# Kernel optimization log

Measured on AMD Instinct MI355X. Metric: run time of the kernel, lower is better.

## Reference

```python
import jax, jax.numpy as jnp
import numpy as np
from jax import lax

DIM = 512
HEADS = 8


def _branch(x, w1, wd):
    # 1x1 pointwise conv (no bias)
    y = jnp.einsum('oc,bchw->bohw', w1, x)
    # ReflectionPad2d(2)
    y = jnp.pad(y, ((0, 0), (0, 0), (2, 2), (2, 2)), mode='reflect')
    # depthwise 3x3, dilation 2, valid padding (net: same spatial size)
    y = lax.conv_general_dilated(
        y, wd, window_strides=(1, 1), padding='VALID', rhs_dilation=(2, 2),
        dimension_numbers=('NCHW', 'OIHW', 'NCHW'), feature_group_count=y.shape[1])
    return y


def setup_inputs() -> dict:
    key = jax.random.key(0)
    ks = jax.random.split(key, 8)
    s = 0.02
    style_feat = jax.random.normal(ks[0], (16, DIM, 64, 64), dtype=jnp.float32)
    fw1 = jax.random.normal(ks[1], (DIM, DIM), dtype=jnp.float32) * s
    fwd_ = jax.random.normal(ks[2], (DIM, 1, 3, 3), dtype=jnp.float32) * s
    gw1 = jax.random.normal(ks[3], (DIM, DIM), dtype=jnp.float32) * s
    gwd = jax.random.normal(ks[4], (DIM, 1, 3, 3), dtype=jnp.float32) * s
    hw1 = jax.random.normal(ks[5], (DIM, DIM), dtype=jnp.float32) * s
    hwd = jax.random.normal(ks[6], (DIM, 1, 3, 3), dtype=jnp.float32) * s
    ow = jax.random.normal(ks[7], (DIM, DIM), dtype=jnp.float32) * s
    temperature = jnp.ones((HEADS, 1, 1), dtype=jnp.float32)
    return dict(style_feat=style_feat, fw1=fw1, fwd_=fwd_, gw1=gw1, gwd=gwd,
                hw1=hw1, hwd=hwd, ow=ow, temperature=temperature)


def reference(style_feat, fw1, fwd_, gw1, gwd, hw1, hwd, ow, temperature):
    B, C, H, W = style_feat.shape
    cph = C // HEADS
    f_x = _branch(style_feat, fw1, fwd_)
    g_x = _branch(style_feat, gw1, gwd)
    h_x = _branch(style_feat, hw1, hwd)
    q = f_x.reshape(B, HEADS, cph, H * W)
    k = g_x.reshape(B, HEADS, cph, H * W)
    v = h_x.reshape(B, HEADS, cph, H * W)
    # channel-wise attention: [B,h,cph,cph]
    energy = jnp.einsum('bhcn,bhdn->bhcd', q, k)
    attn = jax.nn.softmax(energy * temperature[None], axis=-1)
    out = jnp.einsum('bhcd,bhdn->bhcn', attn, v).reshape(B, C, H, W)
    out = jnp.einsum('oc,bchw->bohw', ow, out)
    return out + style_feat
```

## Files before the change

kernel.cpp:

```cpp
#include <hip/hip_runtime.h>

typedef unsigned short u16;
typedef __bf16 bf8_t __attribute__((ext_vector_type(8)));
typedef short short8 __attribute__((ext_vector_type(8)));
typedef u16 u16x4 __attribute__((ext_vector_type(4)));
typedef float f32x4 __attribute__((ext_vector_type(4)));

#define DEV __device__ __forceinline__

DEV u16 f2bf(float x) {
  unsigned u = __builtin_bit_cast(unsigned, x);
  return (u16)((u + 0x7FFFu + ((u >> 16) & 1u)) >> 16);
}
DEV float bf2f(u16 x) {
  unsigned u = (unsigned)x << 16;
  return __builtin_bit_cast(float, u);
}

DEV void gload16(const u16* g, u16* l) {
  __builtin_amdgcn_global_load_lds((__attribute__((address_space(1))) void*)(g),
                                   (__attribute__((address_space(3))) void*)(l), 16, 0, 0);
}

__global__ void k_waw(const float* __restrict__ f, const float* __restrict__ g,
                      const float* __restrict__ h, u16* __restrict__ AW) {
  int cid = blockIdx.x * 256 + threadIdx.x;
  int lane = cid & 63, m = (cid >> 6) & 3, wm = (cid >> 8) & 1;
  int kt = (cid >> 9) & 15, mt = cid >> 13;
  int row = mt * 128 + wm * 64 + m * 16 + (lane & 15);
  int col = kt * 32 + (lane >> 4) * 8;
  int t = row >> 9, rr = row & 511;
  const float* src = (t == 0 ? f : t == 1 ? g : h) + (size_t)rr * 512 + col;
  f32x4 v0 = *(const f32x4*)src;
  f32x4 v1 = *(const f32x4*)(src + 4);
  short8 s;
#pragma unroll
  for (int e = 0; e < 4; ++e) { s[e] = (short)f2bf(v0[e]); s[e + 4] = (short)f2bf(v1[e]); }
  *(short8*)(AW + (size_t)cid * 8) = s;
}

__global__ __launch_bounds__(256) void k_xt(const float* __restrict__ style, u16* __restrict__ Xt) {
  __shared__ float t[32][33];
  int b = blockIdx.z, c0 = blockIdx.y * 32, n0 = blockIdx.x * 32;
  int tid = threadIdx.x, lr = tid >> 5, lc = tid & 31;
  const float* src = style + ((size_t)b * 512 + c0) * 4096 + n0;
#pragma unroll
  for (int it = 0; it < 4; ++it) {
    int r = it * 8 + lr;
    t[r][lc] = src[(size_t)r * 4096 + lc];
  }
  __syncthreads();
  u16* dst = Xt + ((size_t)b * 4096 + n0) * 512 + c0;
#pragma unroll
  for (int it = 0; it < 4; ++it) {
    int n = it * 8 + lr;
    dst[(size_t)n * 512 + lc] = f2bf(t[lc][n]);
  }
}

DEV void stage_tile(const u16* __restrict__ src, int row0, int kb,
                    u16* lds, int wave, int lane) {
#pragma unroll
  for (int qq = 0; qq < 2; ++qq) {
    int idx = (wave * 2 + qq) * 64 + lane;
    int r = idx >> 2;
    int cb = (idx & 3) * 8;
    gload16(src + (size_t)(row0 + r) * 512 + (kb + cb),
            lds + (wave * 2 + qq) * 512);
  }
}

__global__ __launch_bounds__(256, 2) void k_gemm_branch(
    const u16* __restrict__ AW, const u16* __restrict__ Xt, u16* __restrict__ Y) {
  int z = blockIdx.z;
  int t = z >> 4, b = z & 15;
  int mt = t * 4 + blockIdx.y;
  int N0 = blockIdx.x * 128;
  const u16* B = Xt + (size_t)b * (4096 * 512);
  u16* C = Y + (size_t)b * (1536 * 4096);
  int tid = threadIdx.x, wave = tid >> 6, lane = tid & 63;
  int wm = wave >> 1, wn = wave & 1;
  __shared__ __align__(16) u16 lB[2][128 * 32];
  f32x4 acc[4][4];
#pragma unroll
  for (int m = 0; m < 4; ++m)
#pragma unroll
    for (int n = 0; n < 4; ++n) acc[m][n] = (f32x4){0.f, 0.f, 0.f, 0.f};
  stage_tile(B, N0, 0, &lB[0][0], wave, lane);
  __syncthreads();
  int lrow = lane & 15, lk = (lane >> 4) * 8;
#pragma unroll 2
  for (int kt = 0; kt < 16; ++kt) {
    int cur = kt & 1;
    if (kt < 15) stage_tile(B, N0, (kt + 1) * 32, &lB[cur ^ 1][0], wave, lane);
    const u16* ab = AW + (size_t)((mt * 16 + kt) * 2 + wm) * 2048 + lane * 8;
    bf8_t af[4], bff[4];
#pragma unroll
    for (int m = 0; m < 4; ++m) af[m] = *(const bf8_t*)(ab + m * 512);
#pragma unroll
    for (int n = 0; n < 4; ++n)
      bff[n] = *(const bf8_t*)&lB[cur][(wn * 64 + n * 16 + lrow) * 32 + lk];
#pragma unroll
    for (int m = 0; m < 4; ++m)
#pragma unroll
      for (int n = 0; n < 4; ++n)
        acc[m][n] = __builtin_amdgcn_mfma_f32_16x16x32_bf16(af[m], bff[n], acc[m][n], 0, 0, 0);
    __syncthreads();
  }
  int orow = (lane >> 4) * 4, ocol = lane & 15;
#pragma unroll
  for (int m = 0; m < 4; ++m)
#pragma unroll
    for (int n = 0; n < 4; ++n) {
      int row = mt * 128 + wm * 64 + m * 16 + orow;
      int col = N0 + wn * 64 + n * 16 + ocol;
      u16* cp = C + (size_t)row * 4096 + col;
#pragma unroll
      for (int i = 0; i < 4; ++i) cp[(size_t)i * 4096] = f2bf(acc[m][n][i]);
    }
}

template <typename F>
DEV void dw_row(const u16* plane, const float* w9, int y, F&& store) {
  short8 raw[3][8];
#pragma unroll
  for (int i = 0; i < 3; ++i) {
    int yy = y + 2 * i - 2;
    yy = yy < 0 ? -yy : (yy > 63 ? 126 - yy : yy);
    const short8* rp = (const short8*)(plane + yy * 64);
#pragma unroll
    for (int ch = 0; ch < 8; ++ch) raw[i][ch] = rp[ch];
  }
#pragma unroll
  for (int g = 0; g < 4; ++g) {
    float fr[3][20];
#pragma unroll
    for (int t = 0; t < 20; ++t) {
      int p = g * 16 - 2 + t;
      int rp2 = p < 0 ? -p : (p > 63 ? 126 - p : p);
#pragma unroll
      for (int i = 0; i < 3; ++i)
        fr[i][t] = bf2f((u16)raw[i][rp2 >> 3][rp2 & 7]);
    }
    float o[16];
#pragma unroll
    for (int e = 0; e < 16; ++e) {
      float s = 0.f;
#pragma unroll
      for (int i = 0; i < 3; ++i)
#pragma unroll
        for (int j = 0; j < 3; ++j)
          s += w9[i * 3 + j] * fr[i][e + 2 * j];
      o[e] = s;
    }
    store(g, o);
  }
}

__global__ __launch_bounds__(256, 2) void k_dwE(const u16* __restrict__ Y,
    const float* __restrict__ fwd, const float* __restrict__ gwd, float* __restrict__ E) {
  int band = blockIdx.x, h = blockIdx.y, b = blockIdx.z;
  __shared__ __align__(16) u16 qbuf[64 * 256];
  __shared__ __align__(16) u16 kbuf[64 * 256];
  int tid = threadIdx.x;
  int c = ((tid >> 5) << 3) | (tid & 7);
  int yl = (tid >> 3) & 3;
  int wv = tid >> 6, lane = tid & 63;
  int lrow = lane & 15, lkg = lane >> 4;
  const u16* qp = Y + ((size_t)b * 1536 + h * 64 + c) * 4096;
  const u16* kp = Y + ((size_t)b * 1536 + 512 + h * 64 + c) * 4096;
  float wq9[9], wk9[9];
#pragma unroll
  for (int t = 0; t < 9; ++t) {
    wq9[t] = fwd[(h * 64 + c) * 9 + t];
    wk9[t] = gwd[(h * 64 + c) * 9 + t];
  }
  f32x4 acc[4];
#pragma unroll
  for (int n = 0; n < 4; ++n) acc[n] = (f32x4){0.f, 0.f, 0.f, 0.f};
  char* qrow = (char*)qbuf + c * 512;
  char* krow = (char*)kbuf + c * 512;
  int c7 = c & 7;
#pragma unroll 1
  for (int sb = 0; sb < 4; ++sb) {
    int y = band * 16 + sb * 4 + yl;
    dw_row(qp, wq9, y, [&](int g, const float* o) {
      short8 s0, s1;
#pragma unroll
      for (int e = 0; e < 8; ++e) { s0[e] = (short)f2bf(o[e]); s1[e] = (short)f2bf(o[e + 8]); }
      int ch0 = yl * 8 + g * 2;
      *(short8*)(qrow + 16 * (ch0 ^ c7)) = s0;
      *(short8*)(qrow + 16 * ((ch0 + 1) ^ c7)) = s1;
    });
    dw_row(kp, wk9, y, [&](int g, const float* o) {
      short8 s0, s1;
#pragma unroll
      for (int e = 0; e < 8; ++e) { s0[e] = (short)f2bf(o[e]); s1[e] = (short)f2bf(o[e + 8]); }
      int ch0 = yl * 8 + g * 2;
      *(short8*)(krow + 16 * (ch0 ^ c7)) = s0;
      *(short8*)(krow + 16 * ((ch0 + 1) ^ c7)) = s1;
    });
    __syncthreads();
    const char* qb = (const char*)qbuf + (wv * 16 + lrow) * 512;
    int ca7 = (wv * 16 + lrow) & 7;
#pragma unroll
    for (int ks = 0; ks < 8; ++ks) {
      bf8_t aF = *(const bf8_t*)(qb + 16 * ((ks * 4 + lkg) ^ ca7));
#pragma unroll
      for (int n = 0; n < 4; ++n) {
        int cb = n * 16 + lrow;
        bf8_t bF = *(const bf8_t*)((const char*)kbuf + cb * 512 + 16 * ((ks * 4 + lkg) ^ (cb & 7)));
        acc[n] = __builtin_amdgcn_mfma_f32_16x16x32_bf16(aF, bF, acc[n], 0, 0, 0);
      }
    }
    __syncthreads();
  }
  float* Eo = E + (((size_t)band * 16 + b) * 8 + h) * 4096;
  int orow = (lane >> 4) * 4, ocol = lane & 15;
#pragma unroll
  for (int n = 0; n < 4; ++n)
#pragma unroll
    for (int i = 0; i < 4; ++i)
      Eo[(wv * 16 + orow + i) * 64 + n * 16 + ocol] = acc[n][i];
}

__global__ __launch_bounds__(256, 2) void k_dwV(const u16* __restrict__ Y,
    const float* __restrict__ hwd, u16* __restrict__ Vt) {
  int band = blockIdx.x, ct = blockIdx.y, b = blockIdx.z;
  __shared__ float vb[256 * 68];
  int tid = threadIdx.x;
  int c = ((tid >> 5) << 3) | (tid & 7);
  int yl = (tid >> 3) & 3;
  int cg = tid & 7;
  int cglob = ct * 64 + c;
  const u16* plane = Y + ((size_t)b * 1536 + 1024 + cglob) * 4096;
  float w9[9];
#pragma unroll
  for (int t = 0; t < 9; ++t) w9[t] = hwd[cglob * 9 + t];
#pragma unroll 1
  for (int sb = 0; sb < 4; ++sb) {
    int y = band * 16 + sb * 4 + yl;
    dw_row(plane, w9, y, [&](int g, const float* o) {
#pragma unroll
      for (int e = 0; e < 16; ++e)
        vb[((g * 16 + e) * 4 + yl) * 68 + c] = o[e];
    });
    __syncthreads();
#pragma unroll
    for (int k = 0; k < 8; ++k) {
      int np = (tid >> 3) + 32 * k;
      int x = np >> 2, yy = np & 3;
      int ng = (band * 16 + sb * 4 + yy) * 64 + x;
      f32x4 r0 = *(const f32x4*)&vb[np * 68 + cg * 8];
      f32x4 r1 = *(const f32x4*)&vb[np * 68 + cg * 8 + 4];
      short8 s;
#pragma unroll
      for (int e = 0; e < 4; ++e) { s[e] = (short)f2bf(r0[e]); s[e + 4] = (short)f2bf(r1[e]); }
      *(short8*)(Vt + ((size_t)b * 4096 + ng) * 512 + ct * 64 + cg * 8) = s;
    }
    __syncthreads();
  }
}

__global__ __launch_bounds__(64) void k_softmax(float* __restrict__ E, const float* __restrict__ temp) {
  int bh = blockIdx.x;
  int b = bh >> 3, h = bh & 7;
  int c = threadIdx.x;
  float* p0 = E + (((size_t)b * 8 + h) * 64 + c) * 64;
  float tv = temp[h];
  float e[64];
  float mx = -1e30f;
#pragma unroll
  for (int d = 0; d < 64; ++d) {
    float v = (p0[d] + p0[d + 524288] + p0[d + 1048576] + p0[d + 1572864]) * tv;
    e[d] = v;
    mx = fmaxf(mx, v);
  }
  float s = 0.f;
#pragma unroll
  for (int d = 0; d < 64; ++d) { float v = __expf(e[d] - mx); e[d] = v; s += v; }
  float inv = 1.f / s;
#pragma unroll
  for (int d = 0; d < 64; ++d) p0[d] = e[d] * inv;
}

__global__ __launch_bounds__(256) void k_m2(const float* __restrict__ E, const float* __restrict__ ow,
                                            u16* __restrict__ M2) {
  int og = blockIdx.x, h = blockIdx.y, b = blockIdx.z;
  __shared__ float at[4096];
  int tid = threadIdx.x;
  const float* attn = E + ((size_t)b * 8 + h) * 4096;
  for (int v = tid; v < 4096; v += 256) at[v] = attn[v];
  __syncthreads();
  int o = og * 64 + (tid >> 2), dq = (tid & 3) * 16;
  const float* owr = ow + (size_t)o * 512 + h * 64;
  float acc[16];
#pragma unroll
  for (int e = 0; e < 16; ++e) acc[e] = 0.f;
  for (int cc = 0; cc < 64; ++cc) {
    float wv = owr[cc];
#pragma unroll
    for (int e = 0; e < 16; ++e) acc[e] += wv * at[cc * 64 + dq + e];
  }
  u16* dst = M2 + ((size_t)b * 512 + o) * 512 + h * 64 + dq;
  short8 s0, s1;
#pragma unroll
  for (int e = 0; e < 8; ++e) { s0[e] = (short)f2bf(acc[e]); s1[e] = (short)f2bf(acc[e + 8]); }
  *(short8*)dst = s0;
  *(short8*)(dst + 8) = s1;
}

DEV void stage_tile_f(const u16* __restrict__ src, int row0, int kb,
                      u16* lds, int wave, int lane) {
#pragma unroll
  for (int qq = 0; qq < 2; ++qq) {
    int idx = (wave * 2 + qq) * 64 + lane;
    int r = idx >> 2;
    int cb = (idx & 3) * 8;
    gload16(src + (size_t)(row0 + r) * 512 + (kb + cb),
            lds + (wave * 2 + qq) * 512);
  }
}

__global__ __launch_bounds__(256, 2) void k_gemm_final(
    const u16* __restrict__ M2, const u16* __restrict__ Vt,
    const float* __restrict__ style, float* __restrict__ out) {
  int b = blockIdx.z;
  const u16* A = M2 + (size_t)b * (512 * 512);
  const u16* B = Vt + (size_t)b * (4096 * 512);
  const float* st = style + (size_t)b * (512 * 4096);
  float* op = out + (size_t)b * (512 * 4096);
  int M0 = blockIdx.y * 128, N0 = blockIdx.x * 128;
  int tid = threadIdx.x, wave = tid >> 6, lane = tid & 63;
  int wm = wave >> 1, wn = wave & 1;
  __shared__ __align__(16) u16 lA[2][128 * 32];
  __shared__ __align__(16) u16 lB[2][128 * 32];
  f32x4 acc[4][4];
#pragma unroll
  for (int m = 0; m < 4; ++m)
#pragma unroll
    for (int n = 0; n < 4; ++n) acc[m][n] = (f32x4){0.f, 0.f, 0.f, 0.f};
  stage_tile_f(A, M0, 0, &lA[0][0], wave, lane);
  stage_tile_f(B, N0, 0, &lB[0][0], wave, lane);
  __syncthreads();
  int lrow = lane & 15, lk = (lane >> 4) * 8;
#pragma unroll 2
  for (int kt = 0; kt < 16; ++kt) {
    int cur = kt & 1;
    if (kt < 15) {
      stage_tile_f(A, M0, (kt + 1) * 32, &lA[cur ^ 1][0], wave, lane);
      stage_tile_f(B, N0, (kt + 1) * 32, &lB[cur ^ 1][0], wave, lane);
    }
    bf8_t af[4], bff[4];
#pragma unroll
    for (int m = 0; m < 4; ++m)
      af[m] = *(const bf8_t*)&lA[cur][(wm * 64 + m * 16 + lrow) * 32 + lk];
#pragma unroll
    for (int n = 0; n < 4; ++n)
      bff[n] = *(const bf8_t*)&lB[cur][(wn * 64 + n * 16 + lrow) * 32 + lk];
#pragma unroll
    for (int m = 0; m < 4; ++m)
#pragma unroll
      for (int n = 0; n < 4; ++n)
        acc[m][n] = __builtin_amdgcn_mfma_f32_16x16x32_bf16(af[m], bff[n], acc[m][n], 0, 0, 0);
    __syncthreads();
  }
  int orow = (lane >> 4) * 4, ocol = lane & 15;
#pragma unroll
  for (int m = 0; m < 4; ++m)
#pragma unroll
    for (int n = 0; n < 4; ++n) {
      int row = M0 + wm * 64 + m * 16 + orow;
      int col = N0 + wn * 64 + n * 16 + ocol;
      float* cp = op + (size_t)row * 4096 + col;
      const float* sp = st + (size_t)row * 4096 + col;
#pragma unroll
      for (int i = 0; i < 4; ++i) cp[(size_t)i * 4096] = acc[m][n][i] + sp[(size_t)i * 4096];
    }
}


extern "C" void kernel_launch(void* const* d_in, const int* in_sizes, int n_in,
                              void* d_out, int out_size, void* d_ws, size_t ws_size,
                              hipStream_t stream) {
  const float* style = (const float*)d_in[0];
  const float* fw1   = (const float*)d_in[1];
  const float* fwd_  = (const float*)d_in[2];
  const float* gw1   = (const float*)d_in[3];
  const float* gwd   = (const float*)d_in[4];
  const float* hw1   = (const float*)d_in[5];
  const float* hwd   = (const float*)d_in[6];
  const float* ow    = (const float*)d_in[7];
  const float* temp  = (const float*)d_in[8];
  float* out = (float*)d_out;

  char* ws = (char*)d_ws;
  u16*   AW  = (u16*)(ws + 0);
  u16*   Y   = (u16*)(ws + (size_t)2097152);
  u16*   Xt  = (u16*)(ws + (size_t)203423744);
  u16*   Vt  = Xt;
  float* E   = (float*)(ws + (size_t)270532608);
  u16*   M2  = (u16*)(ws + (size_t)278921216);

  k_waw<<<384, 256, 0, stream>>>(fw1, gw1, hw1, AW);
  k_xt<<<dim3(128, 16, 16), 256, 0, stream>>>(style, Xt);
  k_gemm_branch<<<dim3(32, 4, 48), 256, 0, stream>>>(AW, Xt, Y);
  k_dwE<<<dim3(4, 8, 16), 256, 0, stream>>>(Y, fwd_, gwd, E);
  k_dwV<<<dim3(4, 8, 16), 256, 0, stream>>>(Y, hwd, Vt);
  k_softmax<<<128, 64, 0, stream>>>(E, temp);
  k_m2<<<dim3(8, 8, 16), 256, 0, stream>>>(E, ow, M2);
  k_gemm_final<<<dim3(32, 4, 16), 256, 0, stream>>>(M2, Vt, style, out);
}
```

Measured before the change: 413.4 us.

## Stage GEMM epilogue through LDS and fuse dw/softmax kernels

The branch GEMM epilogue now writes its accumulators into a swizzled LDS tile and stores 16-byte coalesced rows, where before it issued scattered 2-byte global stores. The QK-energy and V depthwise kernels are merged into one launch selected by blockIdx.y, so the two sets of blocks run together. Softmax is folded into the M2 kernel, which recomputes the softmax for each output-group block, removing one launch and an E round trip. In exchange, the softmax work is repeated 8 times, the epilogue adds LDS use and barriers, and the larger shared footprint may reduce occupancy.

```diff
diff --git a/kernel.cpp b/kernel.cpp
--- a/kernel.cpp
+++ b/kernel.cpp
@@ -81,6 +81,7 @@
   int tid = threadIdx.x, wave = tid >> 6, lane = tid & 63;
   int wm = wave >> 1, wn = wave & 1;
   __shared__ __align__(16) u16 lB[2][128 * 32];
+  __shared__ __align__(16) u16 Cs[64 * 128];
   f32x4 acc[4][4];
 #pragma unroll
   for (int m = 0; m < 4; ++m)
@@ -109,15 +110,28 @@
   }
   int orow = (lane >> 4) * 4, ocol = lane & 15;
 #pragma unroll
-  for (int m = 0; m < 4; ++m)
-#pragma unroll
-    for (int n = 0; n < 4; ++n) {
-      int row = mt * 128 + wm * 64 + m * 16 + orow;
-      int col = N0 + wn * 64 + n * 16 + ocol;
-      u16* cp = C + (size_t)row * 4096 + col;
-#pragma unroll
-      for (int i = 0; i < 4; ++i) cp[(size_t)i * 4096] = f2bf(acc[m][n][i]);
-    }
+  for (int half = 0; half < 2; ++half) {
+    if (wm == half) {
+#pragma unroll
+      for (int m = 0; m < 4; ++m)
+#pragma unroll
+        for (int n = 0; n < 4; ++n)
+#pragma unroll
+          for (int i = 0; i < 4; ++i) {
+            int r = m * 16 + orow + i;
+            int cph = wn * 64 + n * 16 + ocol;
+            Cs[r * 128 + (((cph >> 3) ^ (r & 15)) << 3) + (cph & 7)] = f2bf(acc[m][n][i]);
+          }
+    }
+    __syncthreads();
+#pragma unroll
+    for (int p = 0; p < 4; ++p) {
+      int r2 = p * 16 + (tid >> 4), g2 = tid & 15;
+      short8 v = *(const short8*)&Cs[r2 * 128 + ((g2 ^ (r2 & 15)) << 3)];
+      *(short8*)(C + (size_t)(mt * 128 + half * 64 + r2) * 4096 + N0 + g2 * 8) = v;
+    }
+    if (half == 0) __syncthreads();
+  }
 }
 
 template <typename F>
@@ -157,140 +171,136 @@
   }
 }
 
-__global__ __launch_bounds__(256, 2) void k_dwE(const u16* __restrict__ Y,
-    const float* __restrict__ fwd, const float* __restrict__ gwd, float* __restrict__ E) {
-  int band = blockIdx.x, h = blockIdx.y, b = blockIdx.z;
-  __shared__ __align__(16) u16 qbuf[64 * 256];
-  __shared__ __align__(16) u16 kbuf[64 * 256];
+__global__ __launch_bounds__(256, 2) void k_dw2(const u16* __restrict__ Y,
+    const float* __restrict__ fwd, const float* __restrict__ gwd,
+    const float* __restrict__ hwd, float* __restrict__ E, u16* __restrict__ Vt) {
+  __shared__ __align__(16) char smem[69632];
+  int band = blockIdx.x, b = blockIdx.z;
   int tid = threadIdx.x;
-  int c = ((tid >> 5) << 3) | (tid & 7);
-  int yl = (tid >> 3) & 3;
-  int wv = tid >> 6, lane = tid & 63;
-  int lrow = lane & 15, lkg = lane >> 4;
-  const u16* qp = Y + ((size_t)b * 1536 + h * 64 + c) * 4096;
-  const u16* kp = Y + ((size_t)b * 1536 + 512 + h * 64 + c) * 4096;
-  float wq9[9], wk9[9];
-#pragma unroll
-  for (int t = 0; t < 9; ++t) {
-    wq9[t] = fwd[(h * 64 + c) * 9 + t];
-    wk9[t] = gwd[(h * 64 + c) * 9 + t];
-  }
-  f32x4 acc[4];
-#pragma unroll
-  for (int n = 0; n < 4; ++n) acc[n] = (f32x4){0.f, 0.f, 0.f, 0.f};
-  char* qrow = (char*)qbuf + c * 512;
-  char* krow = (char*)kbuf + c * 512;
-  int c7 = c & 7;
+  if (blockIdx.y < 8) {
+    int h = blockIdx.y;
+    u16* qbuf = (u16*)smem;
+    u16* kbuf = (u16*)(smem + 32768);
+    int c = ((tid >> 5) << 3) | (tid & 7);
+    int yl = (tid >> 3) & 3;
+    int wv = tid >> 6, lane = tid & 63;
+    int lrow = lane & 15, lkg = lane >> 4;
+    const u16* qp = Y + ((size_t)b * 1536 + h * 64 + c) * 4096;
+    const u16* kp = Y + ((size_t)b * 1536 + 512 + h * 64 + c) * 4096;
+    float wq9[9], wk9[9];
+#pragma unroll
+    for (int t = 0; t < 9; ++t) {
+      wq9[t] = fwd[(h * 64 + c) * 9 + t];
+      wk9[t] = gwd[(h * 64 + c) * 9 + t];
+    }
+    f32x4 acc[4];
+#pragma unroll
+    for (int n = 0; n < 4; ++n) acc[n] = (f32x4){0.f, 0.f, 0.f, 0.f};
+    char* qrow = (char*)qbuf + c * 512;
+    char* krow = (char*)kbuf + c * 512;
+    int c7 = c & 7;
 #pragma unroll 1
-  for (int sb = 0; sb < 4; ++sb) {
-    int y = band * 16 + sb * 4 + yl;
-    dw_row(qp, wq9, y, [&](int g, const float* o) {
-      short8 s0, s1;
-#pragma unroll
-      for (int e = 0; e < 8; ++e) { s0[e] = (short)f2bf(o[e]); s1[e] = (short)f2bf(o[e + 8]); }
-      int ch0 = yl * 8 + g * 2;
-      *(short8*)(qrow + 16 * (ch0 ^ c7)) = s0;
-      *(short8*)(qrow + 16 * ((ch0 + 1) ^ c7)) = s1;
-    });
-    dw_row(kp, wk9, y, [&](int g, const float* o) {
-      short8 s0, s1;
-#pragma unroll
-      for (int e = 0; e < 8; ++e) { s0[e] = (short)f2bf(o[e]); s1[e] = (short)f2bf(o[e + 8]); }
-      int ch0 = yl * 8 + g * 2;
-      *(short8*)(krow + 16 * (ch0 ^ c7)) = s0;
-      *(short8*)(krow + 16 * ((ch0 + 1) ^ c7)) = s1;
-    });
-    __syncthreads();
-    const char* qb = (const char*)qbuf + (wv * 16 + lrow) * 512;
-    int ca7 = (wv * 16 + lrow) & 7;
-#pragma unroll
-    for (int ks = 0; ks < 8; ++ks) {
-      bf8_t aF = *(const bf8_t*)(qb + 16 * ((ks * 4 + lkg) ^ ca7));
-#pragma unroll
-      for (int n = 0; n < 4; ++n) {
-        int cb = n * 16 + lrow;
-        bf8_t bF = *(const bf8_t*)((const char*)kbuf + cb * 512 + 16 * ((ks * 4 + lkg) ^ (cb & 7)));
-        acc[n] = __builtin_amdgcn_mfma_f32_16x16x32_bf16(aF, bF, acc[n], 0, 0, 0);
+    for (int sb = 0; sb < 4; ++sb) {
+      int y = band * 16 + sb * 4 + yl;
+      dw_row(qp, wq9, y, [&](int g, const float* o) {
+        short8 s0, s1;
+#pragma unroll
+        for (int e = 0; e < 8; ++e) { s0[e] = (short)f2bf(o[e]); s1[e] = (short)f2bf(o[e + 8]); }
+        int ch0 = yl * 8 + g * 2;
+        *(short8*)(qrow + 16 * (ch0 ^ c7)) = s0;
+        *(short8*)(qrow + 16 * ((ch0 + 1) ^ c7)) = s1;
+      });
+      dw_row(kp, wk9, y, [&](int g, const float* o) {
+        short8 s0, s1;
+#pragma unroll
+        for (int e = 0; e < 8; ++e) { s0[e] = (short)f2bf(o[e]); s1[e] = (short)f2bf(o[e + 8]); }
+        int ch0 = yl * 8 + g * 2;
+        *(short8*)(krow + 16 * (ch0 ^ c7)) = s0;
+        *(short8*)(krow + 16 * ((ch0 + 1) ^ c7)) = s1;
+      });
+      __syncthreads();
+      const char* qb = (const char*)qbuf + (wv * 16 + lrow) * 512;
+      int ca7 = (wv * 16 + lrow) & 7;
+#pragma unroll
+      for (int ks = 0; ks < 8; ++ks) {
+        bf8_t aF = *(const bf8_t*)(qb + 16 * ((ks * 4 + lkg) ^ ca7));
+#pragma unroll
+        for (int n = 0; n < 4; ++n) {
+          int cb = n * 16 + lrow;
+          bf8_t bF = *(const bf8_t*)((const char*)kbuf + cb * 512 + 16 * ((ks * 4 + lkg) ^ (cb & 7)));
+          acc[n] = __builtin_amdgcn_mfma_f32_16x16x32_bf16(aF, bF, acc[n], 0, 0, 0);
+        }
       }
-    }
-    __syncthreads();
-  }
-  float* Eo = E + (((size_t)band * 16 + b) * 8 + h) * 4096;
-  int orow = (lane >> 4) * 4, ocol = lane & 15;
-#pragma unroll
-  for (int n = 0; n < 4; ++n)
-#pragma unroll
-    for (int i = 0; i < 4; ++i)
-      Eo[(wv * 16 + orow + i) * 64 + n * 16 + ocol] = acc[n][i];
-}
-
-__global__ __launch_bounds__(256, 2) void k_dwV(const u16* __restrict__ Y,
-    const float* __restrict__ hwd, u16* __restrict__ Vt) {
-  int band = blockIdx.x, ct = blockIdx.y, b = blockIdx.z;
-  __shared__ float vb[256 * 68];
-  int tid = threadIdx.x;
-  int c = ((tid >> 5) << 3) | (tid & 7);
-  int yl = (tid >> 3) & 3;
-  int cg = tid & 7;
-  int cglob = ct * 64 + c;
-  const u16* plane = Y + ((size_t)b * 1536 + 1024 + cglob) * 4096;
-  float w9[9];
-#pragma unroll
-  for (int t = 0; t < 9; ++t) w9[t] = hwd[cglob * 9 + t];
+      __syncthreads();
+    }
+    float* Eo = E + (((size_t)band * 16 + b) * 8 + h) * 4096;
+    int orow = (lane >> 4) * 4, ocol = lane & 15;
+#pragma unroll
+    for (int n = 0; n < 4; ++n)
+#pragma unroll
+      for (int i = 0; i < 4; ++i)
+        Eo[(wv * 16 + orow + i) * 64 + n * 16 + ocol] = acc[n][i];
+  } else {
+    int ct = blockIdx.y - 8;
+    float* vb = (float*)smem;
+    int c = ((tid >> 5) << 3) | (tid & 7);
+    int yl = (tid >> 3) & 3;
+    int cg = tid & 7;
+    int cglob = ct * 64 + c;
+    const u16* plane = Y + ((size_t)b * 1536 + 1024 + cglob) * 4096;
+    float w9[9];
+#pragma unroll
+    for (int t = 0; t < 9; ++t) w9[t] = hwd[cglob * 9 + t];
 #pragma unroll 1
-  for (int sb = 0; sb < 4; ++sb) {
-    int y = band * 16 + sb * 4 + yl;
-    dw_row(plane, w9, y, [&](int g, const float* o) {
-#pragma unroll
-      for (int e = 0; e < 16; ++e)
-        vb[((g * 16 + e) * 4 + yl) * 68 + c] = o[e];
-    });
-    __syncthreads();
-#pragma unroll
-    for (int k = 0; k < 8; ++k) {
-      int np = (tid >> 3) + 32 * k;
-      int x = np >> 2, yy = np & 3;
-      int ng = (band * 16 + sb * 4 + yy) * 64 + x;
-      f32x4 r0 = *(const f32x4*)&vb[np * 68 + cg * 8];
-      f32x4 r1 = *(const f32x4*)&vb[np * 68 + cg * 8 + 4];
-      short8 s;
-#pragma unroll
-      for (int e = 0; e < 4; ++e) { s[e] = (short)f2bf(r0[e]); s[e + 4] = (short)f2bf(r1[e]); }
-      *(short8*)(Vt + ((size_t)b * 4096 + ng) * 512 + ct * 64 + cg * 8) = s;
-    }
-    __syncthreads();
-  }
-}
-
-__global__ __launch_bounds__(64) void k_softmax(float* __restrict__ E, const float* __restrict__ temp) {
-  int bh = blockIdx.x;
-  int b = bh >> 3, h = bh & 7;
-  int c = threadIdx.x;
-  float* p0 = E + (((size_t)b * 8 + h) * 64 + c) * 64;
-  float tv = temp[h];
-  float e[64];
-  float mx = -1e30f;
-#pragma unroll
-  for (int d = 0; d < 64; ++d) {
-    float v = (p0[d] + p0[d + 524288] + p0[d + 1048576] + p0[d + 1572864]) * tv;
-    e[d] = v;
-    mx = fmaxf(mx, v);
-  }
-  float s = 0.f;
-#pragma unroll
-  for (int d = 0; d < 64; ++d) { float v = __expf(e[d] - mx); e[d] = v; s += v; }
-  float inv = 1.f / s;
-#pragma unroll
-  for (int d = 0; d < 64; ++d) p0[d] = e[d] * inv;
-}
-
-__global__ __launch_bounds__(256) void k_m2(const float* __restrict__ E, const float* __restrict__ ow,
-                                            u16* __restrict__ M2) {
+    for (int sb = 0; sb < 4; ++sb) {
+      int y = band * 16 + sb * 4 + yl;
+      dw_row(plane, w9, y, [&](int g, const float* o) {
+#pragma unroll
+        for (int e = 0; e < 16; ++e)
+          vb[((g * 16 + e) * 4 + yl) * 68 + c] = o[e];
+      });
+      __syncthreads();
+#pragma unroll
+      for (int k = 0; k < 8; ++k) {
+        int np = (tid >> 3) + 32 * k;
+        int x = np >> 2, yy = np & 3;
+        int ng = (band * 16 + sb * 4 + yy) * 64 + x;
+        f32x4 r0 = *(const f32x4*)&vb[np * 68 + cg * 8];
+        f32x4 r1 = *(const f32x4*)&vb[np * 68 + cg * 8 + 4];
+        short8 s;
+#pragma unroll
+        for (int e = 0; e < 4; ++e) { s[e] = (short)f2bf(r0[e]); s[e + 4] = (short)f2bf(r1[e]); }
+        *(short8*)(Vt + ((size_t)b * 4096 + ng) * 512 + ct * 64 + cg * 8) = s;
+      }
+      __syncthreads();
+    }
+  }
+}
+
+__global__ __launch_bounds__(256) void k_sm2(const float* __restrict__ E,
+    const float* __restrict__ temp, const float* __restrict__ ow, u16* __restrict__ M2) {
   int og = blockIdx.x, h = blockIdx.y, b = blockIdx.z;
   __shared__ float at[4096];
   int tid = threadIdx.x;
-  const float* attn = E + ((size_t)b * 8 + h) * 4096;
-  for (int v = tid; v < 4096; v += 256) at[v] = attn[v];
+  if (tid < 64) {
+    int c = tid;
+    const float* pr = E + (((size_t)b * 8 + h) * 64 + c) * 64;
+    float tv = temp[h];
+    float e[64];
+    float mx = -1e30f;
+#pragma unroll
+    for (int d = 0; d < 64; ++d) {
+      float v = (pr[d] + pr[d + 524288] + pr[d + 1048576] + pr[d + 1572864]) * tv;
+      e[d] = v;
+      mx = fmaxf(mx, v);
+    }
+    float s = 0.f;
+#pragma unroll
+    for (int d = 0; d < 64; ++d) { float v = __expf(e[d] - mx); e[d] = v; s += v; }
+    float inv = 1.f / s;
+#pragma unroll
+    for (int d = 0; d < 64; ++d) at[c * 64 + d] = e[d] * inv;
+  }
   __syncthreads();
   int o = og * 64 + (tid >> 2), dq = (tid & 3) * 16;
   const float* owr = ow + (size_t)o * 512 + h * 64;
@@ -405,9 +415,7 @@
   k_waw<<<384, 256, 0, stream>>>(fw1, gw1, hw1, AW);
   k_xt<<<dim3(128, 16, 16), 256, 0, stream>>>(style, Xt);
   k_gemm_branch<<<dim3(32, 4, 48), 256, 0, stream>>>(AW, Xt, Y);
-  k_dwE<<<dim3(4, 8, 16), 256, 0, stream>>>(Y, fwd_, gwd, E);
-  k_dwV<<<dim3(4, 8, 16), 256, 0, stream>>>(Y, hwd, Vt);
-  k_softmax<<<128, 64, 0, stream>>>(E, temp);
-  k_m2<<<dim3(8, 8, 16), 256, 0, stream>>>(E, ow, M2);
+  k_dw2<<<dim3(4, 16, 16), 256, 0, stream>>>(Y, fwd_, gwd, hwd, E, Vt);
+  k_sm2<<<dim3(8, 8, 16), 256, 0, stream>>>(E, temp, ow, M2);
   k_gemm_final<<<dim3(32, 4, 16), 256, 0, stream>>>(M2, Vt, style, out);
 }
```

Result: slower. 473.3 us (+14.5%).
